# Kernel optimization log

Hardware: AMD Instinct MI355X
Metric: run time of the kernel (lower is better)

The kernel has to match this reference:

```python
import jax, jax.numpy as jnp
import numpy as np

N, D_IN, D_OUT, RANK, MAX_LORAS = 4096, 2048, 2048, 16, 32


def setup_inputs() -> dict:
    key = jax.random.key(0)
    ks = jax.random.split(key, 6)
    x = jax.random.normal(ks[0], (N, D_IN), dtype=jnp.float32)
    adapter_ids = jax.random.randint(ks[1], (N,), 0, MAX_LORAS, dtype=jnp.int32)
    W_base = jax.random.normal(ks[2], (D_OUT, D_IN), dtype=jnp.float32) * (D_IN ** -0.5)
    b_base = jax.random.normal(ks[3], (D_OUT,), dtype=jnp.float32) * 0.01
    lora_A = jax.random.normal(ks[4], (MAX_LORAS, RANK, D_IN), dtype=jnp.float32) * (D_IN ** -0.5)
    lora_B = jax.random.normal(ks[5], (MAX_LORAS, D_OUT, RANK), dtype=jnp.float32) * (RANK ** -0.5)
    lora_scaling = jnp.ones((MAX_LORAS,), dtype=jnp.float32)
    return {"x": x, "adapter_ids": adapter_ids, "W_base": W_base, "b_base": b_base,
            "lora_A": lora_A, "lora_B": lora_B, "lora_scaling": lora_scaling}


def reference(x, adapter_ids, W_base, b_base, lora_A, lora_B, lora_scaling):
    previous_dtype = x.dtype
    # base_layer(x): dense Linear
    result = x @ W_base.T + b_base                      # [N, D_OUT]
    # lora_A(x, adapter_ids): per-token gathered low-rank down-projection (bgmv)
    A_w = lora_A[adapter_ids]                           # [N, RANK, D_IN]
    A_result = jnp.einsum('ni,nri->nr', x, A_w)         # [N, RANK]
    # lora_B(A_result, adapter_ids): per-token gathered up-projection
    B_w = lora_B[adapter_ids]                           # [N, D_OUT, RANK]
    B_result = jnp.einsum('nr,nor->no', A_result, B_w)  # [N, D_OUT]
    # scaled residual add, per-adapter scaling
    scaling = lora_scaling[adapter_ids][:, None]        # [N, 1]
    result = result + B_result * scaling
    # cast back to input dtype (skip_dtype_convert=False)
    return result.astype(previous_dtype)
```

## Files before the change

### kernel.cpp

```cpp
#include <hip/hip_runtime.h>
#include <hip/hip_bf16.h>
#include <stdint.h>

#define NTOK 4096
#define DIN  2048
#define DOUT 2048
#define RANK 16
#define NLORA 32
#define LCAP 512

typedef __attribute__((ext_vector_type(4))) float f32x4;
typedef __attribute__((ext_vector_type(8))) _Float16 f16x8;
typedef __attribute__((ext_vector_type(4))) _Float16 f16x4;

typedef const __attribute__((address_space(1))) void* gas_ptr;
typedef __attribute__((address_space(3))) void* las_ptr;

__device__ __forceinline__ f16x8 cvt8(const float* p) {
    f32x4 a = *(const f32x4*)(p);
    f32x4 b = *(const f32x4*)(p + 4);
    f16x8 h;
    h[0] = (_Float16)a.x; h[1] = (_Float16)a.y; h[2] = (_Float16)a.z; h[3] = (_Float16)a.w;
    h[4] = (_Float16)b.x; h[5] = (_Float16)b.y; h[6] = (_Float16)b.z; h[7] = (_Float16)b.w;
    return h;
}

__global__ __launch_bounds__(256)
void prep_kernel(const float* __restrict__ x, const int* __restrict__ ids,
                 const float* __restrict__ W, const float* __restrict__ lA,
                 const float* __restrict__ lB,
                 _Float16* __restrict__ xh, _Float16* __restrict__ wh,
                 _Float16* __restrict__ lAh, _Float16* __restrict__ lBh,
                 int* __restrict__ list, int* __restrict__ counts) {
    const int bid = blockIdx.x;
    if (bid < 3584) {
        const float* src; _Float16* dst; int lb;
        if      (bid < 1024) { src = W;  dst = wh;  lb = bid; }
        else if (bid < 3072) { src = x;  dst = xh;  lb = bid - 1024; }
        else if (bid < 3328) { src = lA; dst = lAh; lb = bid - 3072; }
        else                 { src = lB; dst = lBh; lb = bid - 3328; }
        const size_t i = ((size_t)lb * 256 + threadIdx.x) * 16;
        *(f16x8*)(dst + i)     = cvt8(src + i);
        *(f16x8*)(dst + i + 8) = cvt8(src + i + 8);
        return;
    }
    const int a = bid - 3584;
    const int wv = threadIdx.x >> 6;
    const int lane = threadIdx.x & 63;
    __shared__ int wcnt[4];
    int c = 0;
    for (int t0 = wv * 1024; t0 < wv * 1024 + 1024; t0 += 64)
        c += __popcll(__ballot(ids[t0 + lane] == a));
    if (lane == 0) wcnt[wv] = c;
    __syncthreads();
    int off = 0;
    for (int w = 0; w < wv; w++) off += wcnt[w];
    if (threadIdx.x == 0) counts[a] = wcnt[0] + wcnt[1] + wcnt[2] + wcnt[3];
    for (int t0 = wv * 1024; t0 < wv * 1024 + 1024; t0 += 64) {
        const int t = t0 + lane;
        const bool m = (ids[t] == a);
        unsigned long long bal = __ballot(m);
        if (m) {
            int pos = off + __popcll(bal & ((1ULL << lane) - 1));
            if (pos < LCAP) list[a * LCAP + pos] = t;
        }
        off += __popcll(bal);
    }
}

__global__ __launch_bounds__(512)
void lora_kernel(const _Float16* __restrict__ xh, const _Float16* __restrict__ lAh,
                 const _Float16* __restrict__ lBh, const float* __restrict__ bias,
                 const float* __restrict__ scal, const int* __restrict__ list,
                 const int* __restrict__ counts, _Float16* __restrict__ Bresh) {
    const int a = blockIdx.x, tile = blockIdx.y;
    const int cnt = counts[a];
    if (tile * 16 >= cnt) return;
    const int wave = threadIdx.x >> 6;
    const int lane = threadIdx.x & 63;
    const int fr = lane & 15, fq = lane >> 4;

    __shared__ float red[8][256];
    __shared__ _Float16 ares_h[16 * RANK];

    const int idxA = tile * 16 + fr;
    const int tA = (idxA < cnt) ? list[a * LCAP + idxA] : list[a * LCAP];

    const _Float16* xr = xh + (size_t)tA * DIN + wave * 256 + fq * 8;
    const _Float16* ar = lAh + (size_t)a * RANK * DIN + (size_t)fr * DIN + wave * 256 + fq * 8;
    f32x4 acc = (f32x4){0.f, 0.f, 0.f, 0.f};
#pragma unroll
    for (int st = 0; st < 8; st++) {
        f16x8 af = *(const f16x8*)(xr + st * 32);
        f16x8 bf = *(const f16x8*)(ar + st * 32);
        acc = __builtin_amdgcn_mfma_f32_16x16x32_f16(af, bf, acc, 0, 0, 0);
    }
#pragma unroll
    for (int j = 0; j < 4; j++) red[wave][lane * 4 + j] = acc[j];
    __syncthreads();
    if (wave == 0) {
        const float s = scal[a];
#pragma unroll
        for (int j = 0; j < 4; j++) {
            float v = 0.f;
#pragma unroll
            for (int w = 0; w < 8; w++) v += red[w][lane * 4 + j];
            ares_h[(fq * 4 + j) * RANK + fr] = (_Float16)(v * s);
        }
    }
    __syncthreads();

    f16x8 ares_frag = {};
    if (fq < 2) ares_frag = *(const f16x8*)(ares_h + fr * RANK + fq * 8);
    const bool valid = (tile * 16 + fr < cnt);
    const int tok = tA;
    const _Float16* Bb = lBh + (size_t)a * DOUT * RANK;
    _Float16* outrow = Bresh + (size_t)tok * DOUT;

#pragma unroll 4
    for (int oi = 0; oi < 16; oi++) {
        const int ot = wave * 16 + oi;
        f16x8 bfrag = {};
        if (fq < 2) bfrag = *(const f16x8*)(Bb + (size_t)(ot * 16 + fr) * RANK + fq * 8);
        f32x4 c = (f32x4){0.f, 0.f, 0.f, 0.f};
        c = __builtin_amdgcn_mfma_f32_16x16x32_f16(bfrag, ares_frag, c, 0, 0, 0);
        const f32x4 bv = *(const f32x4*)(bias + ot * 16 + fq * 4);
        if (valid) {
            f16x4 o4;
            o4[0] = (_Float16)(c[0] + bv.x);
            o4[1] = (_Float16)(c[1] + bv.y);
            o4[2] = (_Float16)(c[2] + bv.z);
            o4[3] = (_Float16)(c[3] + bv.w);
            *(f16x4*)(outrow + ot * 16 + fq * 4) = o4;
        }
    }
}

#define GBK 64
#define NT (DIN / GBK)

__global__ __launch_bounds__(256, 2)
void gemm_kernel(const _Float16* __restrict__ Ah, const _Float16* __restrict__ Wh,
                 const _Float16* __restrict__ Bresh, float* __restrict__ out) {
    extern __shared__ _Float16 sm[];
    _Float16* As = sm;
    _Float16* Bs = sm + 16384;

    const int tid = threadIdx.x;
    const int wave = tid >> 6;
    const int lane = tid & 63;
    const int wr = wave >> 1, wc = wave & 1;

    const int p = blockIdx.x;
    const int L = (p & 7) * 64 + (p >> 3);
    const int bm = (L >> 4) * 128;
    const int bn = (L & 15) * 128;

    const int rsub = lane >> 3;
    const int cch = (lane & 7) ^ rsub;
    const _Float16* srcA[4];
    const _Float16* srcB[4];
#pragma unroll
    for (int i = 0; i < 4; i++) {
        const int row = (wave * 4 + i) * 8 + rsub;
        srcA[i] = Ah + (size_t)(bm + row) * DIN + cch * 8;
        srcB[i] = Wh + (size_t)(bn + row) * DIN + cch * 8;
    }

    const int fr = lane & 15;
    const int fq = lane >> 4;

    f32x4 acc[4][4];
#pragma unroll
    for (int i = 0; i < 4; i++)
#pragma unroll
        for (int j = 0; j < 4; j++) acc[i][j] = (f32x4){0.f, 0.f, 0.f, 0.f};

#define STAGE(buf, koff)                                                                  \
    do {                                                                                  \
        _Pragma("unroll")                                                                 \
        for (int i = 0; i < 4; i++) {                                                     \
            __builtin_amdgcn_global_load_lds((gas_ptr)(srcA[i] + (koff)),                 \
                (las_ptr)(As + (buf) * 8192 + (wave * 4 + i) * 512), 16, 0, 0);           \
            __builtin_amdgcn_global_load_lds((gas_ptr)(srcB[i] + (koff)),                 \
                (las_ptr)(Bs + (buf) * 8192 + (wave * 4 + i) * 512), 16, 0, 0);           \
        }                                                                                 \
    } while (0)

    STAGE(0, 0);

    for (int kt = 0; kt < NT; ++kt) {
        const int cur = kt & 1;
        if (kt < NT - 1) {
            STAGE(cur ^ 1, (kt + 1) * GBK);
            asm volatile("s_waitcnt vmcnt(8)" ::: "memory");
        } else {
            asm volatile("s_waitcnt vmcnt(0)" ::: "memory");
        }
        __builtin_amdgcn_s_barrier();
        __builtin_amdgcn_sched_barrier(0);

        const _Float16* Ab = As + cur * 8192;
        const _Float16* Bb = Bs + cur * 8192;
#pragma unroll
        for (int kk = 0; kk < 2; kk++) {
            f16x8 av[4], bv[4];
#pragma unroll
            for (int mi = 0; mi < 4; mi++) {
                const int row = wr * 64 + mi * 16 + fr;
                const int slot = (kk * 4 + fq) ^ (row & 7);
                av[mi] = *(const f16x8*)(Ab + row * 64 + slot * 8);
            }
#pragma unroll
            for (int ni = 0; ni < 4; ni++) {
                const int row = wc * 64 + ni * 16 + fr;
                const int slot = (kk * 4 + fq) ^ (row & 7);
                bv[ni] = *(const f16x8*)(Bb + row * 64 + slot * 8);
            }
            __builtin_amdgcn_s_setprio(1);
#pragma unroll
            for (int mi = 0; mi < 4; mi++)
#pragma unroll
                for (int ni = 0; ni < 4; ni++)
                    acc[mi][ni] = __builtin_amdgcn_mfma_f32_16x16x32_f16(av[mi], bv[ni], acc[mi][ni], 0, 0, 0);
            __builtin_amdgcn_s_setprio(0);
        }
        __builtin_amdgcn_s_barrier();
    }

#pragma unroll
    for (int mi = 0; mi < 4; mi++) {
#pragma unroll
        for (int j = 0; j < 4; j++) {
            const int n = bm + wr * 64 + mi * 16 + fq * 4 + j;
#pragma unroll
            for (int ni = 0; ni < 4; ni++) {
                const int o = bn + wc * 64 + ni * 16 + fr;
                out[(size_t)n * DOUT + o] = acc[mi][ni][j] + (float)Bresh[(size_t)n * DOUT + o];
            }
        }
    }
}

extern "C" void kernel_launch(void* const* d_in, const int* in_sizes, int n_in,
                              void* d_out, int out_size, void* d_ws, size_t ws_size,
                              hipStream_t stream) {
    const float* x    = (const float*)d_in[0];
    const int*   ids  = (const int*)d_in[1];
    const float* W    = (const float*)d_in[2];
    const float* bias = (const float*)d_in[3];
    const float* lA   = (const float*)d_in[4];
    const float* lB   = (const float*)d_in[5];
    const float* scal = (const float*)d_in[6];
    float* out = (float*)d_out;

    _Float16* xh    = (_Float16*)d_ws;
    _Float16* wh    = xh + (size_t)NTOK * DIN;
    _Float16* lAh   = wh + (size_t)DOUT * DIN;
    _Float16* lBh   = lAh + (size_t)NLORA * RANK * DIN;
    _Float16* Bresh = lBh + (size_t)NLORA * DOUT * RANK;
    int* list   = (int*)(Bresh + (size_t)NTOK * DOUT);
    int* counts = list + (size_t)NLORA * LCAP;

    prep_kernel<<<dim3(3584 + NLORA), 256, 0, stream>>>(
        x, ids, W, lA, lB, xh, wh, lAh, lBh, list, counts);
    lora_kernel<<<dim3(NLORA, 32), 512, 0, stream>>>(
        xh, lAh, lBh, bias, scal, list, counts, Bresh);
    gemm_kernel<<<dim3(512), 256, 64 * 1024, stream>>>(
        xh, wh, Bresh, out);
}
```

Before: 165.6 us.

## Fuse token bucketing, LoRA compute and fp16 conversion into one kernel

Merges the prep kernel and the LoRA kernel into a single launch. Each LoRA block recomputes its adapter's token bucket in shared memory, which removes the global list/count buffers. LoRA blocks read fp32 lora_A, lora_B and x directly and convert in registers, so the separate lA/lB fp16 conversion passes are gone. Each block handles 32 tokens, as two 16-token MFMA groups. The cost is a redundant scan of the ids array by every LoRA block, and a cap of 256 tokens per adapter: 8 blocks × 32 tokens.

```diff
diff --git a/kernel.cpp b/kernel.cpp
--- a/kernel.cpp
+++ b/kernel.cpp
@@ -7,7 +7,6 @@
 #define DOUT 2048
 #define RANK 16
 #define NLORA 32
-#define LCAP 512
 
 typedef __attribute__((ext_vector_type(4))) float f32x4;
 typedef __attribute__((ext_vector_type(8))) _Float16 f16x8;
@@ -25,113 +24,123 @@
     return h;
 }
 
-__global__ __launch_bounds__(256)
-void prep_kernel(const float* __restrict__ x, const int* __restrict__ ids,
-                 const float* __restrict__ W, const float* __restrict__ lA,
-                 const float* __restrict__ lB,
-                 _Float16* __restrict__ xh, _Float16* __restrict__ wh,
-                 _Float16* __restrict__ lAh, _Float16* __restrict__ lBh,
-                 int* __restrict__ list, int* __restrict__ counts) {
+__global__ __launch_bounds__(512)
+void fused_prep_lora(const float* __restrict__ x, const int* __restrict__ ids,
+                     const float* __restrict__ W, const float* __restrict__ lA,
+                     const float* __restrict__ lB, const float* __restrict__ bias,
+                     const float* __restrict__ scal,
+                     _Float16* __restrict__ xh, _Float16* __restrict__ wh,
+                     _Float16* __restrict__ Bresh) {
     const int bid = blockIdx.x;
-    if (bid < 3584) {
+    const int tid = threadIdx.x;
+    if (bid >= 256) {
         const float* src; _Float16* dst; int lb;
-        if      (bid < 1024) { src = W;  dst = wh;  lb = bid; }
-        else if (bid < 3072) { src = x;  dst = xh;  lb = bid - 1024; }
-        else if (bid < 3328) { src = lA; dst = lAh; lb = bid - 3072; }
-        else                 { src = lB; dst = lBh; lb = bid - 3328; }
-        const size_t i = ((size_t)lb * 256 + threadIdx.x) * 16;
+        if (bid < 768) { src = W; dst = wh; lb = bid - 256; }
+        else           { src = x; dst = xh; lb = bid - 768; }
+        const size_t i = ((size_t)lb * 512 + tid) * 16;
         *(f16x8*)(dst + i)     = cvt8(src + i);
         *(f16x8*)(dst + i + 8) = cvt8(src + i + 8);
         return;
     }
-    const int a = bid - 3584;
-    const int wv = threadIdx.x >> 6;
-    const int lane = threadIdx.x & 63;
-    __shared__ int wcnt[4];
-    int c = 0;
-    for (int t0 = wv * 1024; t0 < wv * 1024 + 1024; t0 += 64)
-        c += __popcll(__ballot(ids[t0 + lane] == a));
-    if (lane == 0) wcnt[wv] = c;
-    __syncthreads();
-    int off = 0;
-    for (int w = 0; w < wv; w++) off += wcnt[w];
-    if (threadIdx.x == 0) counts[a] = wcnt[0] + wcnt[1] + wcnt[2] + wcnt[3];
-    for (int t0 = wv * 1024; t0 < wv * 1024 + 1024; t0 += 64) {
-        const int t = t0 + lane;
+    const int a = bid >> 3, q = bid & 7;
+    const int wv = tid >> 6;
+    const int lane = tid & 63;
+    const int fr = lane & 15, fq = lane >> 4;
+
+    __shared__ int wvcnt[8];
+    __shared__ int toks[32];
+    __shared__ float red[8][2][256];
+    __shared__ _Float16 ares_h[32 * RANK];
+
+    if (tid < 32) toks[tid] = 0;
+    int cw = 0;
+#pragma unroll
+    for (int r = 0; r < 8; r++)
+        cw += __popcll(__ballot(ids[wv * 512 + r * 64 + lane] == a));
+    if (lane == 0) wvcnt[wv] = cw;
+    __syncthreads();
+    int off = 0, cnt = 0;
+#pragma unroll
+    for (int w = 0; w < 8; w++) { if (w < wv) off += wvcnt[w]; cnt += wvcnt[w]; }
+    const int base = q * 32;
+    int run = off;
+#pragma unroll
+    for (int r = 0; r < 8; r++) {
+        const int t = wv * 512 + r * 64 + lane;
         const bool m = (ids[t] == a);
-        unsigned long long bal = __ballot(m);
+        const unsigned long long bal = __ballot(m);
         if (m) {
-            int pos = off + __popcll(bal & ((1ULL << lane) - 1));
-            if (pos < LCAP) list[a * LCAP + pos] = t;
-        }
-        off += __popcll(bal);
-    }
-}
-
-__global__ __launch_bounds__(512)
-void lora_kernel(const _Float16* __restrict__ xh, const _Float16* __restrict__ lAh,
-                 const _Float16* __restrict__ lBh, const float* __restrict__ bias,
-                 const float* __restrict__ scal, const int* __restrict__ list,
-                 const int* __restrict__ counts, _Float16* __restrict__ Bresh) {
-    const int a = blockIdx.x, tile = blockIdx.y;
-    const int cnt = counts[a];
-    if (tile * 16 >= cnt) return;
-    const int wave = threadIdx.x >> 6;
-    const int lane = threadIdx.x & 63;
-    const int fr = lane & 15, fq = lane >> 4;
-
-    __shared__ float red[8][256];
-    __shared__ _Float16 ares_h[16 * RANK];
-
-    const int idxA = tile * 16 + fr;
-    const int tA = (idxA < cnt) ? list[a * LCAP + idxA] : list[a * LCAP];
-
-    const _Float16* xr = xh + (size_t)tA * DIN + wave * 256 + fq * 8;
-    const _Float16* ar = lAh + (size_t)a * RANK * DIN + (size_t)fr * DIN + wave * 256 + fq * 8;
-    f32x4 acc = (f32x4){0.f, 0.f, 0.f, 0.f};
+            const int pos = run + __popcll(bal & ((1ULL << lane) - 1));
+            const int rel = pos - base;
+            if (rel >= 0 && rel < 32) toks[rel] = t;
+        }
+        run += __popcll(bal);
+    }
+    __syncthreads();
+    if (base >= cnt) return;
+
+    const int t0 = toks[fr], t1 = toks[16 + fr];
+    const float* xr0 = x + (size_t)t0 * DIN + wv * 256 + fq * 8;
+    const float* xr1 = x + (size_t)t1 * DIN + wv * 256 + fq * 8;
+    const float* ar = lA + (size_t)a * RANK * DIN + (size_t)fr * DIN + wv * 256 + fq * 8;
+    f32x4 acc0 = (f32x4){0.f, 0.f, 0.f, 0.f};
+    f32x4 acc1 = acc0;
 #pragma unroll
     for (int st = 0; st < 8; st++) {
-        f16x8 af = *(const f16x8*)(xr + st * 32);
-        f16x8 bf = *(const f16x8*)(ar + st * 32);
-        acc = __builtin_amdgcn_mfma_f32_16x16x32_f16(af, bf, acc, 0, 0, 0);
-    }
-#pragma unroll
-    for (int j = 0; j < 4; j++) red[wave][lane * 4 + j] = acc[j];
-    __syncthreads();
-    if (wave == 0) {
+        const f16x8 bf = cvt8(ar + st * 32);
+        acc0 = __builtin_amdgcn_mfma_f32_16x16x32_f16(cvt8(xr0 + st * 32), bf, acc0, 0, 0, 0);
+        acc1 = __builtin_amdgcn_mfma_f32_16x16x32_f16(cvt8(xr1 + st * 32), bf, acc1, 0, 0, 0);
+    }
+#pragma unroll
+    for (int j = 0; j < 4; j++) {
+        red[wv][0][lane * 4 + j] = acc0[j];
+        red[wv][1][lane * 4 + j] = acc1[j];
+    }
+    __syncthreads();
+    if (wv < 2) {
+        const int g = wv;
         const float s = scal[a];
 #pragma unroll
         for (int j = 0; j < 4; j++) {
             float v = 0.f;
 #pragma unroll
-            for (int w = 0; w < 8; w++) v += red[w][lane * 4 + j];
-            ares_h[(fq * 4 + j) * RANK + fr] = (_Float16)(v * s);
-        }
-    }
-    __syncthreads();
-
-    f16x8 ares_frag = {};
-    if (fq < 2) ares_frag = *(const f16x8*)(ares_h + fr * RANK + fq * 8);
-    const bool valid = (tile * 16 + fr < cnt);
-    const int tok = tA;
-    const _Float16* Bb = lBh + (size_t)a * DOUT * RANK;
-    _Float16* outrow = Bresh + (size_t)tok * DOUT;
-
+            for (int w = 0; w < 8; w++) v += red[w][g][lane * 4 + j];
+            ares_h[(g * 16 + fq * 4 + j) * RANK + fr] = (_Float16)(v * s);
+        }
+    }
+    __syncthreads();
+
+    f16x8 aresf[2] = {{}, {}};
+    if (fq < 2) {
+        aresf[0] = *(const f16x8*)(ares_h + (size_t)fr * RANK + fq * 8);
+        aresf[1] = *(const f16x8*)(ares_h + (size_t)(16 + fr) * RANK + fq * 8);
+    }
+    const bool val0 = (base + fr < cnt);
+    const bool val1 = (base + 16 + fr < cnt);
+    const float* Bb = lB + (size_t)a * DOUT * RANK;
+    _Float16* orow0 = Bresh + (size_t)t0 * DOUT;
+    _Float16* orow1 = Bresh + (size_t)t1 * DOUT;
 #pragma unroll 4
     for (int oi = 0; oi < 16; oi++) {
-        const int ot = wave * 16 + oi;
+        const int ot = wv * 16 + oi;
         f16x8 bfrag = {};
-        if (fq < 2) bfrag = *(const f16x8*)(Bb + (size_t)(ot * 16 + fr) * RANK + fq * 8);
-        f32x4 c = (f32x4){0.f, 0.f, 0.f, 0.f};
-        c = __builtin_amdgcn_mfma_f32_16x16x32_f16(bfrag, ares_frag, c, 0, 0, 0);
+        if (fq < 2) bfrag = cvt8(Bb + (size_t)(ot * 16 + fr) * RANK + fq * 8);
+        f32x4 c0 = (f32x4){0.f, 0.f, 0.f, 0.f};
+        f32x4 c1 = c0;
+        c0 = __builtin_amdgcn_mfma_f32_16x16x32_f16(bfrag, aresf[0], c0, 0, 0, 0);
+        c1 = __builtin_amdgcn_mfma_f32_16x16x32_f16(bfrag, aresf[1], c1, 0, 0, 0);
         const f32x4 bv = *(const f32x4*)(bias + ot * 16 + fq * 4);
-        if (valid) {
+        if (val0) {
             f16x4 o4;
-            o4[0] = (_Float16)(c[0] + bv.x);
-            o4[1] = (_Float16)(c[1] + bv.y);
-            o4[2] = (_Float16)(c[2] + bv.z);
-            o4[3] = (_Float16)(c[3] + bv.w);
-            *(f16x4*)(outrow + ot * 16 + fq * 4) = o4;
+            o4[0] = (_Float16)(c0[0] + bv.x); o4[1] = (_Float16)(c0[1] + bv.y);
+            o4[2] = (_Float16)(c0[2] + bv.z); o4[3] = (_Float16)(c0[3] + bv.w);
+            *(f16x4*)(orow0 + ot * 16 + fq * 4) = o4;
+        }
+        if (val1) {
+            f16x4 o4;
+            o4[0] = (_Float16)(c1[0] + bv.x); o4[1] = (_Float16)(c1[1] + bv.y);
+            o4[2] = (_Float16)(c1[2] + bv.z); o4[3] = (_Float16)(c1[3] + bv.w);
+            *(f16x4*)(orow1 + ot * 16 + fq * 4) = o4;
         }
     }
 }
@@ -256,16 +265,10 @@
 
     _Float16* xh    = (_Float16*)d_ws;
     _Float16* wh    = xh + (size_t)NTOK * DIN;
-    _Float16* lAh   = wh + (size_t)DOUT * DIN;
-    _Float16* lBh   = lAh + (size_t)NLORA * RANK * DIN;
-    _Float16* Bresh = lBh + (size_t)NLORA * DOUT * RANK;
-    int* list   = (int*)(Bresh + (size_t)NTOK * DOUT);
-    int* counts = list + (size_t)NLORA * LCAP;
-
-    prep_kernel<<<dim3(3584 + NLORA), 256, 0, stream>>>(
-        x, ids, W, lA, lB, xh, wh, lAh, lBh, list, counts);
-    lora_kernel<<<dim3(NLORA, 32), 512, 0, stream>>>(
-        xh, lAh, lBh, bias, scal, list, counts, Bresh);
+    _Float16* Bresh = wh + (size_t)DOUT * DIN;
+
+    fused_prep_lora<<<dim3(1792), 512, 0, stream>>>(
+        x, ids, W, lA, lB, bias, scal, xh, wh, Bresh);
     gemm_kernel<<<dim3(512), 256, 64 * 1024, stream>>>(
         xh, wh, Bresh, out);
 }
```

Result: slower. 169.3 us (+2.3%).
